# Performance work log

Hardware: AMD Instinct MI355X
Metric: run time of the kernel (lower is better)

The kernel has to match this reference:

```python
import jax, jax.numpy as jnp
import numpy as np

DIM = 192
STATE = 64
B = 8
H = 64
W = 64
EPS_LN = 1e-5
EPS_BN = 1e-5


def _layernorm(x, g, b):
    m = jnp.mean(x, axis=-1, keepdims=True)
    v = jnp.mean((x - m) ** 2, axis=-1, keepdims=True)
    return (x - m) / jnp.sqrt(v + EPS_LN) * g + b


def _linear(x, w, b=None):
    # torch Linear convention: w is [out, in]
    y = jnp.einsum('...i,oi->...o', x, w)
    return y if b is None else y + b


def _parallel_scan(A, Bd, xp):
    # A, Bd, xp: [B, L, S]; h_t = A_t*h_{t-1} + Bd_t*xp_t via log-space cumsum
    A_safe = jnp.clip(A, 0.001, 0.999)
    log_A = jnp.log(A_safe + 1e-10)
    log_cum_A = jnp.cumsum(log_A, axis=1)
    log_cum_A_max = jnp.max(log_cum_A, axis=1, keepdims=True)
    cum_A = jnp.exp(log_cum_A - log_cum_A_max)
    BX = Bd * xp
    # prepend zeros, drop last: normalizer uses cumprod up to t-1
    log_pad = jnp.pad(log_cum_A - log_cum_A_max, ((0, 0), (1, 0), (0, 0)))[:, :-1]
    BX_norm = BX * jnp.exp(-log_pad)
    return jnp.cumsum(BX_norm, axis=1) * cum_A


def _ssm(x, ln_g, ln_b, xp_w, xp_b, dt_w, dt_b, A_log, B_w, C_w, Dp, out_w, out_b):
    xn = _layernorm(x, ln_g, ln_b)
    delta = jax.nn.softplus(_linear(xn, dt_w, dt_b)) * 0.01 + 0.0001  # [B,L,S]
    B_t = _linear(xn, B_w)
    C_t = _linear(xn, C_w)
    A = -jnp.exp(A_log)  # [S]
    x_proj = _linear(xn, xp_w, xp_b)
    deltaA = jnp.clip(delta * A, -10.0, -0.0001)
    A_disc = jnp.exp(deltaA)
    B_disc = delta * B_t
    h = _parallel_scan(A_disc, B_disc, x_proj)
    y = C_t * h
    y = jnp.where(jnp.all(jnp.isfinite(y)), y, jnp.zeros_like(y))
    y = _linear(y, out_w, out_b)
    return y + jnp.clip(Dp, -2.0, 2.0) * x


def reference(x, ln1_g, ln1_b, ln2_g, ln2_b, dw_w, bn_g, bn_b, bn_rm, bn_rv,
              ssm_ln_g, ssm_ln_b, xp_w, xp_b, dt_w, dt_b, A_log, B_w, C_w,
              D_param, out_w, out_b, mlp_w1, mlp_b1, mlp_w2, mlp_b2,
              alpha_local, alpha_ssm, alpha_mlp):
    identity = x
    # depthwise 3x3 conv + BatchNorm2d (eval mode, running stats)
    xc = jax.lax.conv_general_dilated(
        x, dw_w, (1, 1), 'SAME', feature_group_count=DIM,
        dimension_numbers=('NCHW', 'OIHW', 'NCHW'))
    scale = (bn_g / jnp.sqrt(bn_rv + EPS_BN))[None, :, None, None]
    x_local = (xc - bn_rm[None, :, None, None]) * scale + bn_b[None, :, None, None]
    # SSM branch on flattened spatial sequence
    x_seq = x.transpose(0, 2, 3, 1).reshape(B, H * W, DIM)
    x_seq = _layernorm(x_seq, ln1_g, ln1_b)
    x_seq = _ssm(x_seq, ssm_ln_g, ssm_ln_b, xp_w, xp_b, dt_w, dt_b, A_log,
                 B_w, C_w, D_param, out_w, out_b)
    x_ssm = x_seq.reshape(B, H, W, DIM).transpose(0, 3, 1, 2)
    xr = identity + alpha_local * x_local + alpha_ssm * x_ssm
    # residual MLP (dropout = identity at inference)
    x_mlp = xr.transpose(0, 2, 3, 1).reshape(B, H * W, DIM)
    x_mlp = _layernorm(x_mlp, ln2_g, ln2_b)
    x_mlp = _linear(jax.nn.gelu(_linear(x_mlp, mlp_w1, mlp_b1), approximate=False),
                    mlp_w2, mlp_b2)
    return xr + alpha_mlp * x_mlp.reshape(B, H, W, DIM).transpose(0, 3, 1, 2)


def setup_inputs() -> dict:
    key = jax.random.key(0)
    ks = jax.random.split(key, 12)
    def nrm(k, shape, s):
        return jax.random.normal(k, shape, jnp.float32) * s
    f32 = jnp.float32
    return {
        'x': jax.random.normal(ks[0], (B, DIM, H, W), f32),
        'ln1_g': jnp.ones(DIM, f32), 'ln1_b': jnp.zeros(DIM, f32),
        'ln2_g': jnp.ones(DIM, f32), 'ln2_b': jnp.zeros(DIM, f32),
        'dw_w': nrm(ks[1], (DIM, 1, 3, 3), 0.2),
        'bn_g': jnp.ones(DIM, f32), 'bn_b': jnp.zeros(DIM, f32),
        'bn_rm': jnp.zeros(DIM, f32), 'bn_rv': jnp.ones(DIM, f32),
        'ssm_ln_g': jnp.ones(DIM, f32), 'ssm_ln_b': jnp.zeros(DIM, f32),
        'xp_w': nrm(ks[2], (STATE, DIM), 0.05), 'xp_b': jnp.zeros(STATE, f32),
        'dt_w': nrm(ks[3], (STATE, DIM), 0.05), 'dt_b': jnp.zeros(STATE, f32),
        'A_log': jnp.log(jax.random.uniform(ks[4], (STATE,), f32) * 0.8 + 0.2),
        'B_w': nrm(ks[5], (STATE, DIM), 0.05),
        'C_w': nrm(ks[6], (STATE, DIM), 0.05),
        'D_param': jnp.zeros(DIM, f32),
        'out_w': nrm(ks[7], (DIM, STATE), 0.05), 'out_b': jnp.zeros(DIM, f32),
        'mlp_w1': nrm(ks[8], (4 * DIM, DIM), 0.03), 'mlp_b1': jnp.zeros(4 * DIM, f32),
        'mlp_w2': nrm(ks[9], (DIM, 4 * DIM), 0.03), 'mlp_b2': jnp.zeros(DIM, f32),
        'alpha_local': jnp.full((1,), 0.5, f32),
        'alpha_ssm': jnp.full((1,), 0.5, f32),
        'alpha_mlp': jnp.full((1,), 0.5, f32),
    }
```

## Files before the change

kernel.cpp:

```cpp
#include <hip/hip_runtime.h>
#include <hip/hip_bf16.h>
#include <math.h>


#define DEV static __device__ __forceinline__

constexpr int Bn = 8, Dm = 192, Ln = 4096, Sn = 64, Hd = 768;

typedef __attribute__((ext_vector_type(8))) short bf16x8;
typedef __attribute__((ext_vector_type(4))) float f32x4;

DEV float wave_sum(float v) {
#pragma unroll
  for (int off = 1; off < 64; off <<= 1) v += __shfl_xor(v, off);
  return v;
}

DEV short f2b(float x) {
  __hip_bfloat16 h = __float2bfloat16(x);
  return *(short*)&h;
}

DEV float b2f(short x) {
  __hip_bfloat16 h = *(__hip_bfloat16*)&x;
  return __bfloat162float(h);
}

__global__ __launch_bounds__(256) void k_prep(
    const float* __restrict__ x, const float* __restrict__ g1, const float* __restrict__ b1,
    const float* __restrict__ g2, const float* __restrict__ b2,
    short* __restrict__ xnb, short* __restrict__ xln1b,
    const float* __restrict__ dt_w, const float* __restrict__ B_w,
    const float* __restrict__ C_w, const float* __restrict__ xp_w,
    const float* __restrict__ out_w, const float* __restrict__ w1,
    const float* __restrict__ w2, short* __restrict__ wb) {
  __shared__ __align__(16) float tile[Dm * 65];
  int tid = threadIdx.x;
  if (blockIdx.y == 8) {
    for (int i = blockIdx.x * 256 + tid; i < 89088; i += 64 * 256) {
      const float4* src;
      if (i < 3072)       src = (const float4*)dt_w + i;
      else if (i < 6144)  src = (const float4*)B_w + (i - 3072);
      else if (i < 9216)  src = (const float4*)C_w + (i - 6144);
      else if (i < 12288) src = (const float4*)xp_w + (i - 9216);
      else if (i < 15360) src = (const float4*)out_w + (i - 12288);
      else if (i < 52224) src = (const float4*)w1 + (i - 15360);
      else                src = (const float4*)w2 + (i - 52224);
      float4 v = *src;
      int o = i * 4;
      wb[o] = f2b(v.x); wb[o + 1] = f2b(v.y); wb[o + 2] = f2b(v.z); wb[o + 3] = f2b(v.w);
    }
    return;
  }
  int b = blockIdx.y, l0 = blockIdx.x * 64;
  const float* xb = x + (size_t)b * Dm * Ln;
  for (int i = tid; i < Dm * 16; i += 256) {
    int d = i >> 4, l4 = (i & 15) << 2;
    float4 v = *(const float4*)&xb[d * Ln + l0 + l4];
    tile[d * 65 + l4]     = v.x; tile[d * 65 + l4 + 1] = v.y;
    tile[d * 65 + l4 + 2] = v.z; tile[d * 65 + l4 + 3] = v.w;
  }
  __syncthreads();
  int lane = tid & 63, wv = tid >> 6;
  float ga0 = g1[lane], ga1 = g1[lane + 64], ga2 = g1[lane + 128];
  float bb0 = b1[lane], bb1 = b1[lane + 64], bb2 = b1[lane + 128];
  float gc0 = g2[lane], gc1 = g2[lane + 64], gc2 = g2[lane + 128];
  float bc0 = b2[lane], bc1 = b2[lane + 64], bc2 = b2[lane + 128];
  for (int li = wv; li < 64; li += 4) {
    float v0 = tile[lane * 65 + li], v1 = tile[(lane + 64) * 65 + li], v2 = tile[(lane + 128) * 65 + li];
    float s  = wave_sum(v0 + v1 + v2);
    float sq = wave_sum(v0 * v0 + v1 * v1 + v2 * v2);
    float m = s * (1.f / 192.f);
    float inv = rsqrtf(sq * (1.f / 192.f) - m * m + 1e-5f);
    float y0 = (v0 - m) * inv * ga0 + bb0;
    float y1 = (v1 - m) * inv * ga1 + bb1;
    float y2 = (v2 - m) * inv * ga2 + bb2;
    float s2  = wave_sum(y0 + y1 + y2);
    float sq2 = wave_sum(y0 * y0 + y1 * y1 + y2 * y2);
    float m2 = s2 * (1.f / 192.f);
    float inv2 = rsqrtf(sq2 * (1.f / 192.f) - m2 * m2 + 1e-5f);
    size_t base = ((size_t)b * Ln + l0 + li) * Dm;
    xln1b[base + lane]       = f2b(y0);
    xln1b[base + lane + 64]  = f2b(y1);
    xln1b[base + lane + 128] = f2b(y2);
    xnb[base + lane]       = f2b((y0 - m2) * inv2 * gc0 + bc0);
    xnb[base + lane + 64]  = f2b((y1 - m2) * inv2 * gc1 + bc1);
    xnb[base + lane + 128] = f2b((y2 - m2) * inv2 * gc2 + bc2);
  }
}

__global__ __launch_bounds__(256) void k_proj(
    const short* __restrict__ xnb, const short* __restrict__ wcat,
    const float* __restrict__ dt_b, const float* __restrict__ xp_b,
    const float* __restrict__ A_log, float* __restrict__ aA, unsigned* __restrict__ bxc) {
  __shared__ __align__(16) short As[64 * 72];
  __shared__ __align__(16) short Bs[256 * 72];
  int m0 = blockIdx.x * 64, tid = threadIdx.x;
  int lane = tid & 63, l16 = lane & 15, quad = lane >> 4, w = tid >> 6;
  f32x4 acc[16] = {};
  for (int kt = 0; kt < 3; kt++) {
    int kb = kt * 64;
    for (int i = tid; i < 512; i += 256) {
      int row = i >> 3, c8 = (i & 7) * 8;
      *(float4*)&As[row * 72 + c8] = *(const float4*)&xnb[(size_t)(m0 + row) * 192 + kb + c8];
    }
    for (int i = tid; i < 2048; i += 256) {
      int row = i >> 3, c8 = (i & 7) * 8;
      *(float4*)&Bs[row * 72 + c8] = *(const float4*)&wcat[(size_t)row * 192 + kb + c8];
    }
    __syncthreads();
#pragma unroll
    for (int ks = 0; ks < 2; ks++) {
      int ko = ks * 32 + quad * 8;
      bf16x8 a0 = *(const bf16x8*)&As[(w * 16 + l16) * 72 + ko];
#pragma unroll
      for (int nh = 0; nh < 2; nh++) {
        bf16x8 bfr[8];
#pragma unroll
        for (int j = 0; j < 8; j++) bfr[j] = *(const bf16x8*)&Bs[((nh * 8 + j) * 16 + l16) * 72 + ko];
#pragma unroll
        for (int j = 0; j < 8; j++)
          acc[nh * 8 + j] = __builtin_amdgcn_mfma_f32_16x16x32_bf16(a0, bfr[j], acc[nh * 8 + j], 0, 0, 0);
      }
    }
    __syncthreads();
  }
  float Av[4], dtbv[4], xpbv[4];
#pragma unroll
  for (int ni = 0; ni < 4; ni++) {
    int s = ni * 16 + l16;
    Av[ni] = -expf(A_log[s]); dtbv[ni] = dt_b[s]; xpbv[ni] = xp_b[s];
  }
#pragma unroll
  for (int r = 0; r < 4; r++) {
    int m = m0 + w * 16 + quad * 4 + r;
#pragma unroll
    for (int ni = 0; ni < 4; ni++) {
      int s = ni * 16 + l16;
      float z = acc[ni][r] + dtbv[ni];
      float sp = (z > 20.f) ? z : log1pf(expf(z));
      float delta = sp * 0.01f + 0.0001f;
      float bt  = acc[ni + 4][r];
      float ct  = acc[ni + 8][r];
      float xpv = acc[ni + 12][r] + xpbv[ni];
      float dA = fminf(fmaxf(delta * Av[ni], -10.f), -0.0001f);
      float Ae = fminf(fmaxf(expf(dA), 0.001f), 0.999f) + 1e-10f;
      aA[(size_t)m * 64 + s] = Ae;
      unsigned pk = (unsigned)(unsigned short)f2b(delta * bt * xpv)
                  | ((unsigned)(unsigned short)f2b(ct) << 16);
      bxc[(size_t)m * 64 + s] = pk;
    }
  }
}

__global__ __launch_bounds__(64) void k_scan1(const float* __restrict__ aA,
                                              const unsigned* __restrict__ bxc,
                                              float* __restrict__ sums) {
  int c = blockIdx.x, b = blockIdx.y, s = threadIdx.x;
  size_t r0 = (size_t)b * Ln + c * 32;
  const float* ap = aA + r0 * 64;
  const unsigned* bp = bxc + r0 * 64;
  float prodA = 1.f, h = 0.f;
  int t = 0;
  if (c == 0) { prodA = ap[s]; h = b2f((short)(bp[s] & 0xFFFF)); t = 1; }
#pragma unroll 4
  for (; t < 32; t++) {
    float a = ap[t * 64 + s];
    float bx = b2f((short)(bp[t * 64 + s] & 0xFFFF));
    h = a * (h + bx);
    prodA *= a;
  }
  int ci = b * 128 + c;
  sums[(ci * 2 + 0) * 64 + s] = prodA;
  sums[(ci * 2 + 1) * 64 + s] = h;
}

__global__ __launch_bounds__(64) void k_scan2(const float* __restrict__ sums, float* __restrict__ carries) {
  int b = blockIdx.x, s = threadIdx.x;
  float cur = 0.f;
#pragma unroll 4
  for (int c = 0; c < 128; c++) {
    int ci = b * 128 + c;
    carries[ci * 64 + s] = cur;
    cur = sums[(ci * 2 + 0) * 64 + s] * cur + sums[(ci * 2 + 1) * 64 + s];
  }
}

__global__ __launch_bounds__(64) void k_scan3(const float* __restrict__ aA,
                                              const unsigned* __restrict__ bxc,
                                              const float* __restrict__ carries,
                                              short* __restrict__ y) {
  int c = blockIdx.x, b = blockIdx.y, s = threadIdx.x;
  size_t r0 = (size_t)b * Ln + c * 32;
  const float* ap = aA + r0 * 64;
  const unsigned* bp = bxc + r0 * 64;
  short* yo = y + r0 * 64;
  float h = carries[(b * 128 + c) * 64 + s];
  int t = 0;
  if (c == 0) {
    unsigned u = bp[s];
    h = b2f((short)(u & 0xFFFF));
    yo[s] = f2b(b2f((short)(u >> 16)) * h);
    t = 1;
  }
#pragma unroll 4
  for (; t < 32; t++) {
    unsigned u = bp[t * 64 + s];
    float a = ap[t * 64 + s];
    h = a * (h + b2f((short)(u & 0xFFFF)));
    yo[t * 64 + s] = f2b(b2f((short)(u >> 16)) * h);
  }
}

__global__ __launch_bounds__(256) void k_out(
    const short* __restrict__ y, const short* __restrict__ owb, const float* __restrict__ out_b,
    const float* __restrict__ Dp, const short* __restrict__ xln1b, float* __restrict__ sout) {
  __shared__ __align__(16) short As[96 * 72];
  __shared__ __align__(16) short Bs[64 * 72];
  int l0g = blockIdx.x * 64, d0 = blockIdx.y * 96, tid = threadIdx.x;
  int lane = tid & 63, l16 = lane & 15, quad = lane >> 4;
  int wm = (tid >> 6) >> 1, wn = (tid >> 6) & 1;
  f32x4 acc[3][2] = {};
  for (int i = tid; i < 768; i += 256) {
    int row = i >> 3, c8 = (i & 7) * 8;
    *(float4*)&As[row * 72 + c8] = *(const float4*)&owb[(d0 + row) * 64 + c8];
  }
  for (int i = tid; i < 512; i += 256) {
    int row = i >> 3, c8 = (i & 7) * 8;
    *(float4*)&Bs[row * 72 + c8] = *(const float4*)&y[(size_t)(l0g + row) * 64 + c8];
  }
  __syncthreads();
#pragma unroll
  for (int ks = 0; ks < 2; ks++) {
    int ko = ks * 32 + quad * 8;
    bf16x8 a[3], b[2];
#pragma unroll
    for (int mi = 0; mi < 3; mi++) a[mi] = *(const bf16x8*)&As[(wm * 48 + mi * 16 + l16) * 72 + ko];
#pragma unroll
    for (int ni = 0; ni < 2; ni++) b[ni] = *(const bf16x8*)&Bs[(wn * 32 + ni * 16 + l16) * 72 + ko];
#pragma unroll
    for (int mi = 0; mi < 3; mi++)
#pragma unroll
      for (int ni = 0; ni < 2; ni++)
        acc[mi][ni] = __builtin_amdgcn_mfma_f32_16x16x32_bf16(a[mi], b[ni], acc[mi][ni], 0, 0, 0);
  }
  int bb = l0g >> 12;
#pragma unroll
  for (int mi = 0; mi < 3; mi++)
#pragma unroll
    for (int r = 0; r < 4; r++) {
      int d = d0 + wm * 48 + mi * 16 + quad * 4 + r;
      float ob = out_b[d];
      float dc = fminf(fmaxf(Dp[d], -2.f), 2.f);
#pragma unroll
      for (int ni = 0; ni < 2; ni++) {
        int l = l0g + wn * 32 + ni * 16 + l16;
        float v = acc[mi][ni][r] + ob;
        if (dc != 0.f) v += dc * b2f(xln1b[(size_t)l * 192 + d]);
        sout[((size_t)bb * Dm + d) * Ln + (l & 4095)] = v;
      }
    }
}

__global__ __launch_bounds__(256) void k_conv(
    const float* __restrict__ x, const float* __restrict__ dw,
    const float* __restrict__ bn_g, const float* __restrict__ bn_b,
    const float* __restrict__ bn_rm, const float* __restrict__ bn_rv,
    const float* __restrict__ sout, const float* __restrict__ a_loc,
    const float* __restrict__ a_ssm, float* __restrict__ xr) {
  __shared__ __align__(16) float xs[64 * 64];
  int d = blockIdx.x, b = blockIdx.y, tid = threadIdx.x;
  const float* xp = x + ((size_t)b * Dm + d) * Ln;
  for (int i = tid; i < 1024; i += 256) ((float4*)xs)[i] = ((const float4*)xp)[i];
  __syncthreads();
  float w[9];
#pragma unroll
  for (int k = 0; k < 9; k++) w[k] = dw[d * 9 + k];
  float scale = bn_g[d] * rsqrtf(bn_rv[d] + 1e-5f);
  float rm = bn_rm[d], bb = bn_b[d];
  float al = a_loc[0], as_ = a_ssm[0];
  const float* sp = sout + ((size_t)b * Dm + d) * Ln;
  float* xo = xr + ((size_t)b * Dm + d) * Ln;
  for (int i = tid; i < 4096; i += 256) {
    int h = i >> 6, wc = i & 63;
    float acc = 0.f;
#pragma unroll
    for (int kh = 0; kh < 3; kh++) {
      int hh = h + kh - 1;
      if (hh < 0 || hh >= 64) continue;
#pragma unroll
      for (int kw = 0; kw < 3; kw++) {
        int ww2 = wc + kw - 1;
        if (ww2 < 0 || ww2 >= 64) continue;
        acc += xs[hh * 64 + ww2] * w[kh * 3 + kw];
      }
    }
    float xl = (acc - rm) * scale + bb;
    xo[i] = xs[i] + al * xl + as_ * sp[i];
  }
}

__global__ __launch_bounds__(256) void k_ln2(
    const float* __restrict__ xr, const float* __restrict__ g, const float* __restrict__ bb,
    short* __restrict__ xn2) {
  __shared__ __align__(16) float tile[Dm * 65];
  int b = blockIdx.y, l0 = blockIdx.x * 64, tid = threadIdx.x;
  const float* xb = xr + (size_t)b * Dm * Ln;
  for (int i = tid; i < Dm * 16; i += 256) {
    int d = i >> 4, l4 = (i & 15) << 2;
    float4 v = *(const float4*)&xb[d * Ln + l0 + l4];
    tile[d * 65 + l4]     = v.x; tile[d * 65 + l4 + 1] = v.y;
    tile[d * 65 + l4 + 2] = v.z; tile[d * 65 + l4 + 3] = v.w;
  }
  __syncthreads();
  int lane = tid & 63, wv = tid >> 6;
  float g0 = g[lane], g1v = g[lane + 64], g2v = g[lane + 128];
  float b0 = bb[lane], b1v = bb[lane + 64], b2v = bb[lane + 128];
  for (int li = wv; li < 64; li += 4) {
    float v0 = tile[lane * 65 + li], v1 = tile[(lane + 64) * 65 + li], v2 = tile[(lane + 128) * 65 + li];
    float s  = wave_sum(v0 + v1 + v2);
    float sq = wave_sum(v0 * v0 + v1 * v1 + v2 * v2);
    float m = s * (1.f / 192.f);
    float inv = rsqrtf(sq * (1.f / 192.f) - m * m + 1e-5f);
    size_t base = ((size_t)b * Ln + l0 + li) * Dm;
    xn2[base + lane]       = f2b((v0 - m) * inv * g0 + b0);
    xn2[base + lane + 64]  = f2b((v1 - m) * inv * g1v + b1v);
    xn2[base + lane + 128] = f2b((v2 - m) * inv * g2v + b2v);
  }
}

__global__ __launch_bounds__(256) void k_gemm1(
    const short* __restrict__ xn2, const short* __restrict__ w1b,
    const float* __restrict__ b1h, short* __restrict__ hid) {
  __shared__ __align__(16) short smem[2 * 128 * 88];
  short* As = smem;
  short* Bs = smem + 128 * 88;
  int m0 = blockIdx.x * 128, n0 = blockIdx.y * 128, tid = threadIdx.x;
  int lane = tid & 63, l16 = lane & 15, quad = lane >> 4;
  int wm = (tid >> 6) >> 1, wn = (tid >> 6) & 1;
  f32x4 acc[4][4] = {};
  for (int kt = 0; kt < 3; kt++) {
    int kb = kt * 64;
    for (int i = tid; i < 1024; i += 256) {
      int row = i >> 3, c8 = (i & 7) * 8;
      *(float4*)&As[row * 88 + c8] = *(const float4*)&xn2[(size_t)(m0 + row) * 192 + kb + c8];
      *(float4*)&Bs[row * 88 + c8] = *(const float4*)&w1b[(size_t)(n0 + row) * 192 + kb + c8];
    }
    __syncthreads();
#pragma unroll
    for (int ks = 0; ks < 2; ks++) {
      int ko = ks * 32 + quad * 8;
      bf16x8 a[4], b[4];
#pragma unroll
      for (int mi = 0; mi < 4; mi++) a[mi] = *(const bf16x8*)&As[(wm * 64 + mi * 16 + l16) * 88 + ko];
#pragma unroll
      for (int ni = 0; ni < 4; ni++) b[ni] = *(const bf16x8*)&Bs[(wn * 64 + ni * 16 + l16) * 88 + ko];
#pragma unroll
      for (int mi = 0; mi < 4; mi++)
#pragma unroll
        for (int ni = 0; ni < 4; ni++)
          acc[mi][ni] = __builtin_amdgcn_mfma_f32_16x16x32_bf16(a[mi], b[ni], acc[mi][ni], 0, 0, 0);
    }
    __syncthreads();
  }
  short* Cs = smem;
  float bias4[4];
#pragma unroll
  for (int ni = 0; ni < 4; ni++) bias4[ni] = b1h[n0 + wn * 64 + ni * 16 + l16];
#pragma unroll
  for (int mi = 0; mi < 4; mi++)
#pragma unroll
    for (int ni = 0; ni < 4; ni++) {
      int n = wn * 64 + ni * 16 + l16;
#pragma unroll
      for (int r = 0; r < 4; r++) {
        int m = wm * 64 + mi * 16 + quad * 4 + r;
        float v = acc[mi][ni][r] + bias4[ni];
        float g = 0.5f * v * (1.f + erff(v * 0.70710678118f));
        Cs[m * 136 + n] = f2b(g);
      }
    }
  __syncthreads();
  for (int i = tid; i < 2048; i += 256) {
    int m = i >> 4, ch = i & 15;
    *(float4*)&hid[(size_t)(m0 + m) * 768 + n0 + ch * 8] = *(const float4*)&Cs[m * 136 + ch * 8];
  }
}

__global__ __launch_bounds__(256) void k_gemm2(
    const short* __restrict__ hid, const short* __restrict__ w2b,
    const float* __restrict__ b2o, const float* __restrict__ xr,
    const float* __restrict__ am, float* __restrict__ out) {
  __shared__ __align__(16) short Wt[96 * 88];
  __shared__ __align__(16) short Ht[64 * 88];
  int l0g = blockIdx.x * 64, d0 = blockIdx.y * 96, tid = threadIdx.x;
  int lane = tid & 63, l16 = lane & 15, quad = lane >> 4;
  int wm = (tid >> 6) >> 1, wn = (tid >> 6) & 1;
  f32x4 acc[3][2] = {};
  for (int kt = 0; kt < 12; kt++) {
    int kb = kt * 64;
    for (int i = tid; i < 768; i += 256) {
      int row = i >> 3, c8 = (i & 7) * 8;
      *(float4*)&Wt[row * 88 + c8] = *(const float4*)&w2b[(size_t)(d0 + row) * 768 + kb + c8];
    }
    for (int i = tid; i < 512; i += 256) {
      int row = i >> 3, c8 = (i & 7) * 8;
      *(float4*)&Ht[row * 88 + c8] = *(const float4*)&hid[(size_t)(l0g + row) * 768 + kb + c8];
    }
    __syncthreads();
#pragma unroll
    for (int ks = 0; ks < 2; ks++) {
      int ko = ks * 32 + quad * 8;
      bf16x8 a[3], b[2];
#pragma unroll
      for (int mi = 0; mi < 3; mi++) a[mi] = *(const bf16x8*)&Wt[(wm * 48 + mi * 16 + l16) * 88 + ko];
#pragma unroll
      for (int ni = 0; ni < 2; ni++) b[ni] = *(const bf16x8*)&Ht[(wn * 32 + ni * 16 + l16) * 88 + ko];
#pragma unroll
      for (int mi = 0; mi < 3; mi++)
#pragma unroll
        for (int ni = 0; ni < 2; ni++)
          acc[mi][ni] = __builtin_amdgcn_mfma_f32_16x16x32_bf16(a[mi], b[ni], acc[mi][ni], 0, 0, 0);
    }
    __syncthreads();
  }
  float alpha = am[0];
#pragma unroll
  for (int mi = 0; mi < 3; mi++)
#pragma unroll
    for (int r = 0; r < 4; r++) {
      int d = d0 + wm * 48 + mi * 16 + quad * 4 + r;
      float bias = b2o[d];
#pragma unroll
      for (int ni = 0; ni < 2; ni++) {
        int lg = l0g + wn * 32 + ni * 16 + l16;
        size_t idx = ((size_t)(lg >> 12) * Dm + d) * Ln + (lg & 4095);
        out[idx] = xr[idx] + alpha * (acc[mi][ni][r] + bias);
      }
    }
}

extern "C" void kernel_launch(void* const* d_in, const int* in_sizes, int n_in,
                              void* d_out, int out_size, void* d_ws, size_t ws_size,
                              hipStream_t stream) {
  (void)in_sizes; (void)n_in; (void)out_size; (void)ws_size;
  const float* x     = (const float*)d_in[0];
  const float* ln1_g = (const float*)d_in[1];
  const float* ln1_b = (const float*)d_in[2];
  const float* ln2_g = (const float*)d_in[3];
  const float* ln2_b = (const float*)d_in[4];
  const float* dw_w  = (const float*)d_in[5];
  const float* bn_g  = (const float*)d_in[6];
  const float* bn_b  = (const float*)d_in[7];
  const float* bn_rm = (const float*)d_in[8];
  const float* bn_rv = (const float*)d_in[9];
  const float* ssm_g = (const float*)d_in[10];
  const float* ssm_b = (const float*)d_in[11];
  const float* xp_w  = (const float*)d_in[12];
  const float* xp_b  = (const float*)d_in[13];
  const float* dt_w  = (const float*)d_in[14];
  const float* dt_b  = (const float*)d_in[15];
  const float* A_log = (const float*)d_in[16];
  const float* B_w   = (const float*)d_in[17];
  const float* C_w   = (const float*)d_in[18];
  const float* Dp    = (const float*)d_in[19];
  const float* out_w = (const float*)d_in[20];
  const float* out_b = (const float*)d_in[21];
  const float* w1    = (const float*)d_in[22];
  const float* b1    = (const float*)d_in[23];
  const float* w2    = (const float*)d_in[24];
  const float* b2    = (const float*)d_in[25];
  const float* a_loc = (const float*)d_in[26];
  const float* a_ssm = (const float*)d_in[27];
  const float* a_mlp = (const float*)d_in[28];

  float* ws = (float*)d_ws;
  short*    xnb   = (short*)ws;
  short*    xln1b = (short*)(ws + 3145728);
  float*    aA    = ws + 6291456;
  unsigned* bxc   = (unsigned*)(ws + 8388608);
  short*    yB    = (short*)(ws + 10485760);
  float*    sout  = ws + 11534336;
  float*    xr    = ws + 17825792;
  short*    wb    = (short*)(ws + 24117248);
  float*    sums  = ws + 24829952;
  float*    carr  = ws + 24961024;
  short*    xn2   = (short*)(ws + 25026560);
  short*    hid   = (short*)(ws + 28172288);
  short*    wcatb = wb;
  short*    owb   = wb + 49152;
  short*    w1b   = wb + 61440;
  short*    w2b   = wb + 208896;
  float*    out   = (float*)d_out;

  k_prep <<<dim3(64, 9),  256, 0, stream>>>(x, ln1_g, ln1_b, ssm_g, ssm_b, xnb, xln1b,
                                            dt_w, B_w, C_w, xp_w, out_w, w1, w2, wb);
  k_proj <<<dim3(512),    256, 0, stream>>>(xnb, wcatb, dt_b, xp_b, A_log, aA, bxc);
  k_scan1<<<dim3(128, 8),  64, 0, stream>>>(aA, bxc, sums);
  k_scan2<<<dim3(8),       64, 0, stream>>>(sums, carr);
  k_scan3<<<dim3(128, 8),  64, 0, stream>>>(aA, bxc, carr, yB);
  k_out  <<<dim3(512, 2), 256, 0, stream>>>(yB, owb, out_b, Dp, xln1b, sout);
  k_conv <<<dim3(192, 8), 256, 0, stream>>>(x, dw_w, bn_g, bn_b, bn_rm, bn_rv, sout, a_loc, a_ssm, xr);
  k_ln2  <<<dim3(64, 8),  256, 0, stream>>>(xr, ln2_g, ln2_b, xn2);
  k_gemm1<<<dim3(256, 6), 256, 0, stream>>>(xn2, w1b, b1, hid);
  k_gemm2<<<dim3(512, 2), 256, 0, stream>>>(hid, w2b, b2, xr, a_mlp, out);
}
```

Before: 291.0 us.

## Fuse scan phases into projection and output GEMM kernels, parallelize carry scan

Moves the chunk-level scan reduction (scan1) into the projection kernel's epilogue using shared memory, and fuses the scan finalization (scan3) into the output GEMM so y is produced in LDS without a global round trip. The carry-propagation kernel now uses 4 waves per batch with a two-level scan instead of a single serial wave. This cuts two kernel launches and the global y buffer traffic. In exchange, only 2 of the 4 waves in k_out do the serial scan while the others wait, and k_out now covers all 192 output rows per block with half as many blocks.

```diff
diff --git a/kernel.cpp b/kernel.cpp
--- a/kernel.cpp
+++ b/kernel.cpp
@@ -92,7 +92,8 @@
 __global__ __launch_bounds__(256) void k_proj(
     const short* __restrict__ xnb, const short* __restrict__ wcat,
     const float* __restrict__ dt_b, const float* __restrict__ xp_b,
-    const float* __restrict__ A_log, float* __restrict__ aA, unsigned* __restrict__ bxc) {
+    const float* __restrict__ A_log, float* __restrict__ aA, unsigned* __restrict__ bxc,
+    float* __restrict__ sums) {
   __shared__ __align__(16) short As[64 * 72];
   __shared__ __align__(16) short Bs[256 * 72];
   int m0 = blockIdx.x * 64, tid = threadIdx.x;
@@ -125,6 +126,8 @@
     }
     __syncthreads();
   }
+  float* aAs = (float*)Bs;
+  float* bxs = aAs + 64 * 65;
   float Av[4], dtbv[4], xpbv[4];
 #pragma unroll
   for (int ni = 0; ni < 4; ni++) {
@@ -133,7 +136,8 @@
   }
 #pragma unroll
   for (int r = 0; r < 4; r++) {
-    int m = m0 + w * 16 + quad * 4 + r;
+    int lm = w * 16 + quad * 4 + r;
+    int m = m0 + lm;
 #pragma unroll
     for (int ni = 0; ni < 4; ni++) {
       int s = ni * 16 + l16;
@@ -145,116 +149,127 @@
       float xpv = acc[ni + 12][r] + xpbv[ni];
       float dA = fminf(fmaxf(delta * Av[ni], -10.f), -0.0001f);
       float Ae = fminf(fmaxf(expf(dA), 0.001f), 0.999f) + 1e-10f;
+      short bxh = f2b(delta * bt * xpv);
       aA[(size_t)m * 64 + s] = Ae;
-      unsigned pk = (unsigned)(unsigned short)f2b(delta * bt * xpv)
+      unsigned pk = (unsigned)(unsigned short)bxh
                   | ((unsigned)(unsigned short)f2b(ct) << 16);
       bxc[(size_t)m * 64 + s] = pk;
-    }
-  }
-}
-
-__global__ __launch_bounds__(64) void k_scan1(const float* __restrict__ aA,
-                                              const unsigned* __restrict__ bxc,
-                                              float* __restrict__ sums) {
-  int c = blockIdx.x, b = blockIdx.y, s = threadIdx.x;
-  size_t r0 = (size_t)b * Ln + c * 32;
-  const float* ap = aA + r0 * 64;
-  const unsigned* bp = bxc + r0 * 64;
-  float prodA = 1.f, h = 0.f;
-  int t = 0;
-  if (c == 0) { prodA = ap[s]; h = b2f((short)(bp[s] & 0xFFFF)); t = 1; }
+      aAs[lm * 65 + s] = Ae;
+      bxs[lm * 65 + s] = b2f(bxh);
+    }
+  }
+  __syncthreads();
+  int s = tid & 63, seg = tid >> 6, chunk = seg >> 1, sub = seg & 1;
+  bool first = ((m0 & 4095) == 0) && (chunk == 0) && (sub == 0);
+  float P = 1.f, H = 0.f;
+  int base = chunk * 32 + sub * 16;
+#pragma unroll
+  for (int j = 0; j < 16; j++) {
+    float a  = aAs[(base + j) * 65 + s];
+    float bx = bxs[(base + j) * 65 + s];
+    if (first && j == 0) { P = a; H = bx; }
+    else { P *= a; H = a * (H + bx); }
+  }
+  float* partP = (float*)As;
+  float* partH = partP + 256;
+  partP[seg * 64 + s] = P; partH[seg * 64 + s] = H;
+  __syncthreads();
+  if (tid < 128) {
+    int c = tid >> 6;
+    float p0 = partP[(c * 2) * 64 + s], p1 = partP[(c * 2 + 1) * 64 + s];
+    float h0 = partH[(c * 2) * 64 + s], h1 = partH[(c * 2 + 1) * 64 + s];
+    int ci = (m0 >> 12) * 128 + ((m0 & 4095) >> 5) + c;
+    sums[(ci * 2 + 0) * 64 + s] = p0 * p1;
+    sums[(ci * 2 + 1) * 64 + s] = p1 * h0 + h1;
+  }
+}
+
+__global__ __launch_bounds__(256) void k_scan2(const float* __restrict__ sums,
+                                               float* __restrict__ carries) {
+  __shared__ float Pp[4 * 64], Hp[4 * 64];
+  int b = blockIdx.x, tid = threadIdx.x, s = tid & 63, q = tid >> 6;
+  float P = 1.f, H = 0.f;
 #pragma unroll 4
-  for (; t < 32; t++) {
-    float a = ap[t * 64 + s];
-    float bx = b2f((short)(bp[t * 64 + s] & 0xFFFF));
-    h = a * (h + bx);
-    prodA *= a;
-  }
-  int ci = b * 128 + c;
-  sums[(ci * 2 + 0) * 64 + s] = prodA;
-  sums[(ci * 2 + 1) * 64 + s] = h;
-}
-
-__global__ __launch_bounds__(64) void k_scan2(const float* __restrict__ sums, float* __restrict__ carries) {
-  int b = blockIdx.x, s = threadIdx.x;
+  for (int j = 0; j < 32; j++) {
+    int ci = b * 128 + q * 32 + j;
+    float a = sums[(ci * 2 + 0) * 64 + s];
+    float h = sums[(ci * 2 + 1) * 64 + s];
+    P *= a; H = a * H + h;
+  }
+  Pp[q * 64 + s] = P; Hp[q * 64 + s] = H;
+  __syncthreads();
   float cur = 0.f;
+  for (int qq = 0; qq < q; qq++) cur = Pp[qq * 64 + s] * cur + Hp[qq * 64 + s];
 #pragma unroll 4
-  for (int c = 0; c < 128; c++) {
-    int ci = b * 128 + c;
+  for (int j = 0; j < 32; j++) {
+    int ci = b * 128 + q * 32 + j;
     carries[ci * 64 + s] = cur;
-    cur = sums[(ci * 2 + 0) * 64 + s] * cur + sums[(ci * 2 + 1) * 64 + s];
-  }
-}
-
-__global__ __launch_bounds__(64) void k_scan3(const float* __restrict__ aA,
-                                              const unsigned* __restrict__ bxc,
-                                              const float* __restrict__ carries,
-                                              short* __restrict__ y) {
-  int c = blockIdx.x, b = blockIdx.y, s = threadIdx.x;
-  size_t r0 = (size_t)b * Ln + c * 32;
-  const float* ap = aA + r0 * 64;
-  const unsigned* bp = bxc + r0 * 64;
-  short* yo = y + r0 * 64;
-  float h = carries[(b * 128 + c) * 64 + s];
-  int t = 0;
-  if (c == 0) {
-    unsigned u = bp[s];
-    h = b2f((short)(u & 0xFFFF));
-    yo[s] = f2b(b2f((short)(u >> 16)) * h);
-    t = 1;
-  }
+    float a = sums[(ci * 2 + 0) * 64 + s];
+    float h = sums[(ci * 2 + 1) * 64 + s];
+    cur = a * cur + h;
+  }
+}
+
+__global__ __launch_bounds__(256) void k_out(
+    const float* __restrict__ aA, const unsigned* __restrict__ bxc,
+    const float* __restrict__ carries,
+    const short* __restrict__ owb, const float* __restrict__ out_b,
+    const float* __restrict__ Dp, const short* __restrict__ xln1b, float* __restrict__ sout) {
+  __shared__ __align__(16) short As[192 * 72];
+  __shared__ __align__(16) short Bs[64 * 72];
+  int l0g = blockIdx.x * 64, tid = threadIdx.x;
+  int lane = tid & 63, l16 = lane & 15, quad = lane >> 4, wv = tid >> 6;
+  for (int i = tid; i < 1536; i += 256) {
+    int row = i >> 3, c8 = (i & 7) * 8;
+    *(float4*)&As[row * 72 + c8] = *(const float4*)&owb[row * 64 + c8];
+  }
+  int bb = l0g >> 12, c0 = (l0g & 4095) >> 5;
+  if (wv < 2) {
+    int c = c0 + wv, s = lane;
+    float h = carries[(bb * 128 + c) * 64 + s];
+    const float* ap = aA + (size_t)(l0g + wv * 32) * 64;
+    const unsigned* bp = bxc + (size_t)(l0g + wv * 32) * 64;
+    int t = 0;
+    if (c == 0) {
+      unsigned u = bp[s];
+      h = b2f((short)(u & 0xFFFF));
+      Bs[(wv * 32) * 72 + s] = f2b(b2f((short)(u >> 16)) * h);
+      t = 1;
+    }
 #pragma unroll 4
-  for (; t < 32; t++) {
-    unsigned u = bp[t * 64 + s];
-    float a = ap[t * 64 + s];
-    h = a * (h + b2f((short)(u & 0xFFFF)));
-    yo[t * 64 + s] = f2b(b2f((short)(u >> 16)) * h);
-  }
-}
-
-__global__ __launch_bounds__(256) void k_out(
-    const short* __restrict__ y, const short* __restrict__ owb, const float* __restrict__ out_b,
-    const float* __restrict__ Dp, const short* __restrict__ xln1b, float* __restrict__ sout) {
-  __shared__ __align__(16) short As[96 * 72];
-  __shared__ __align__(16) short Bs[64 * 72];
-  int l0g = blockIdx.x * 64, d0 = blockIdx.y * 96, tid = threadIdx.x;
-  int lane = tid & 63, l16 = lane & 15, quad = lane >> 4;
-  int wm = (tid >> 6) >> 1, wn = (tid >> 6) & 1;
-  f32x4 acc[3][2] = {};
-  for (int i = tid; i < 768; i += 256) {
-    int row = i >> 3, c8 = (i & 7) * 8;
-    *(float4*)&As[row * 72 + c8] = *(const float4*)&owb[(d0 + row) * 64 + c8];
-  }
-  for (int i = tid; i < 512; i += 256) {
-    int row = i >> 3, c8 = (i & 7) * 8;
-    *(float4*)&Bs[row * 72 + c8] = *(const float4*)&y[(size_t)(l0g + row) * 64 + c8];
-  }
-  __syncthreads();
+    for (; t < 32; t++) {
+      unsigned u = bp[t * 64 + s];
+      float a = ap[t * 64 + s];
+      h = a * (h + b2f((short)(u & 0xFFFF)));
+      Bs[(wv * 32 + t) * 72 + s] = f2b(b2f((short)(u >> 16)) * h);
+    }
+  }
+  __syncthreads();
+  f32x4 acc[3][4] = {};
 #pragma unroll
   for (int ks = 0; ks < 2; ks++) {
     int ko = ks * 32 + quad * 8;
-    bf16x8 a[3], b[2];
-#pragma unroll
-    for (int mi = 0; mi < 3; mi++) a[mi] = *(const bf16x8*)&As[(wm * 48 + mi * 16 + l16) * 72 + ko];
-#pragma unroll
-    for (int ni = 0; ni < 2; ni++) b[ni] = *(const bf16x8*)&Bs[(wn * 32 + ni * 16 + l16) * 72 + ko];
+    bf16x8 a[3], b[4];
+#pragma unroll
+    for (int mi = 0; mi < 3; mi++) a[mi] = *(const bf16x8*)&As[(wv * 48 + mi * 16 + l16) * 72 + ko];
+#pragma unroll
+    for (int ni = 0; ni < 4; ni++) b[ni] = *(const bf16x8*)&Bs[(ni * 16 + l16) * 72 + ko];
 #pragma unroll
     for (int mi = 0; mi < 3; mi++)
 #pragma unroll
-      for (int ni = 0; ni < 2; ni++)
+      for (int ni = 0; ni < 4; ni++)
         acc[mi][ni] = __builtin_amdgcn_mfma_f32_16x16x32_bf16(a[mi], b[ni], acc[mi][ni], 0, 0, 0);
   }
-  int bb = l0g >> 12;
 #pragma unroll
   for (int mi = 0; mi < 3; mi++)
 #pragma unroll
     for (int r = 0; r < 4; r++) {
-      int d = d0 + wm * 48 + mi * 16 + quad * 4 + r;
+      int d = wv * 48 + mi * 16 + quad * 4 + r;
       float ob = out_b[d];
       float dc = fminf(fmaxf(Dp[d], -2.f), 2.f);
 #pragma unroll
-      for (int ni = 0; ni < 2; ni++) {
-        int l = l0g + wn * 32 + ni * 16 + l16;
+      for (int ni = 0; ni < 4; ni++) {
+        int l = l0g + ni * 16 + l16;
         float v = acc[mi][ni][r] + ob;
         if (dc != 0.f) v += dc * b2f(xln1b[(size_t)l * 192 + d]);
         sout[((size_t)bb * Dm + d) * Ln + (l & 4095)] = v;
@@ -479,7 +494,6 @@
   short*    xln1b = (short*)(ws + 3145728);
   float*    aA    = ws + 6291456;
   unsigned* bxc   = (unsigned*)(ws + 8388608);
-  short*    yB    = (short*)(ws + 10485760);
   float*    sout  = ws + 11534336;
   float*    xr    = ws + 17825792;
   short*    wb    = (short*)(ws + 24117248);
@@ -495,11 +509,9 @@
 
   k_prep <<<dim3(64, 9),  256, 0, stream>>>(x, ln1_g, ln1_b, ssm_g, ssm_b, xnb, xln1b,
                                             dt_w, B_w, C_w, xp_w, out_w, w1, w2, wb);
-  k_proj <<<dim3(512),    256, 0, stream>>>(xnb, wcatb, dt_b, xp_b, A_log, aA, bxc);
-  k_scan1<<<dim3(128, 8),  64, 0, stream>>>(aA, bxc, sums);
-  k_scan2<<<dim3(8),       64, 0, stream>>>(sums, carr);
-  k_scan3<<<dim3(128, 8),  64, 0, stream>>>(aA, bxc, carr, yB);
-  k_out  <<<dim3(512, 2), 256, 0, stream>>>(yB, owb, out_b, Dp, xln1b, sout);
+  k_proj <<<dim3(512),    256, 0, stream>>>(xnb, wcatb, dt_b, xp_b, A_log, aA, bxc, sums);
+  k_scan2<<<dim3(8),      256, 0, stream>>>(sums, carr);
+  k_out  <<<dim3(512),    256, 0, stream>>>(aA, bxc, carr, owb, out_b, Dp, xln1b, sout);
   k_conv <<<dim3(192, 8), 256, 0, stream>>>(x, dw_w, bn_g, bn_b, bn_rm, bn_rv, sout, a_loc, a_ssm, xr);
   k_ln2  <<<dim3(64, 8),  256, 0, stream>>>(xr, ln2_g, ln2_b, xn2);
   k_gemm1<<<dim3(256, 6), 256, 0, stream>>>(xn2, w1b, b1, hid);
```

After: 271.7 us. 1.07x faster.
